# Kernel optimization log

Measured on AMD Instinct MI355X. Metric: run time of the kernel, lower is better.

The kernel has to match this reference:

```python
import jax, jax.numpy as jnp
import numpy as np

B, T, DM, H = 4, 2048, 1024, 16
D = DM // H  # head_dim = 64


def setup_inputs() -> dict:
    key = jax.random.key(0)
    ks = jax.random.split(key, 10)
    s = 0.02
    return {
        "query": jax.random.normal(ks[0], (B, T, DM), jnp.float32),
        "key": jax.random.normal(ks[1], (B, T, DM), jnp.float32),
        "value": jax.random.normal(ks[2], (B, T, DM), jnp.float32),
        "Wq": jax.random.normal(ks[3], (DM, DM), jnp.float32) * s,
        "bq": jnp.zeros((DM,), jnp.float32),
        "Wk": jax.random.normal(ks[4], (DM, DM), jnp.float32) * s,
        "bk": jnp.zeros((DM,), jnp.float32),
        "Wv": jax.random.normal(ks[5], (DM, DM), jnp.float32) * s,
        "bv": jnp.zeros((DM,), jnp.float32),
        "Wo": jax.random.normal(ks[6], (DM, DM), jnp.float32) * s,
        "bo": jnp.zeros((DM,), jnp.float32),
        "gate_w": jax.random.normal(ks[7], (H, D, D), jnp.float32) * s,
        "gate_b": jax.random.normal(ks[8], (H, D), jnp.float32),
    }


def _split_heads(x):
    # (B, T, DM) -> (B, H, T, D)
    b, t, _ = x.shape
    return x.reshape(b, t, H, D).transpose(0, 2, 1, 3)


def reference(query, key, value, Wq, bq, Wk, bk, Wv, bv, Wo, bo, gate_w, gate_b):
    q = _split_heads(query @ Wq + bq)   # (B,H,T,D)
    k = _split_heads(key @ Wk + bk)
    v = _split_heads(value @ Wv + bv)
    scale = 1.0 / jnp.sqrt(jnp.asarray(D, q.dtype))
    scores = jnp.einsum("bhqd,bhkd->bhqk", q, k) * scale  # (B,H,Tq,Tk)
    attn = jax.nn.softmax(scores, axis=-1)
    y = jnp.einsum("bhqk,bhkd->bhqd", attn, v)            # (B,H,T,D)
    # per-head elementwise gating: sigmoid(W_h y + b_h)
    gate = jax.nn.sigmoid(jnp.einsum("bhtd,hde->bhte", y, gate_w) + gate_b[None, :, None, :])
    y = y * gate
    y = y.transpose(0, 2, 1, 3).reshape(y.shape[0], y.shape[2], H * D)  # merge heads
    return y @ Wo + bo
```

## Files before the change

### kernel.cpp

```cpp
#include <hip/hip_runtime.h>
#include <stdint.h>

typedef unsigned short u16;
typedef uint32_t u32;
typedef __attribute__((ext_vector_type(8))) short bf16x8;
typedef __attribute__((ext_vector_type(4))) float f32x4;
typedef __attribute__((ext_vector_type(4))) u32 u32x4;

__device__ __forceinline__ u16 f2b(float x) {
  union { float f; uint32_t u; } v; v.f = x;
  uint32_t u = v.u;
  return (u16)((u + 0x7fffu + ((u >> 16) & 1u)) >> 16);
}

__device__ __forceinline__ float fexp2(float x) {
  float r;
  asm("v_exp_f32 %0, %1" : "=v"(r) : "v"(x));
  return r;
}

__device__ __forceinline__ u32 cvtpk(float lo, float hi) {
  u32 r;
  asm("v_cvt_pk_bf16_f32 %0, %1, %2" : "=v"(r) : "v"(lo), "v"(hi));
  return r;
}

__device__ __forceinline__ void gload_lds16(const void* g, void* l) {
  __builtin_amdgcn_global_load_lds(
      (const __attribute__((address_space(1))) void*)g,
      (__attribute__((address_space(3))) void*)l, 16, 0, 0);
}

__global__ __launch_bounds__(256) void cvt3_f32_bf16(const float* __restrict__ q,
                                                     const float* __restrict__ k,
                                                     const float* __restrict__ v,
                                                     u16* __restrict__ xq,
                                                     u16* __restrict__ xk,
                                                     u16* __restrict__ xv, int n4) {
  int idx = blockIdx.x * 256 + threadIdx.x;
  if (idx >= n4) return;
  const int z = blockIdx.y;
  const float* in = z == 0 ? q : z == 1 ? k : v;
  u16* out = z == 0 ? xq : z == 1 ? xk : xv;
  float4 vv = ((const float4*)in)[idx];
  ushort4 o;
  o.x = f2b(vv.x); o.y = f2b(vv.y); o.z = f2b(vv.z); o.w = f2b(vv.w);
  ((ushort4*)out)[idx] = o;
}

__global__ __launch_bounds__(256) void transpose_cvt4(const float* __restrict__ w0,
                                                      const float* __restrict__ w1,
                                                      const float* __restrict__ w2,
                                                      const float* __restrict__ w3,
                                                      u16* __restrict__ o0,
                                                      u16* __restrict__ o1,
                                                      u16* __restrict__ o2,
                                                      u16* __restrict__ o3) {
  __shared__ float t[64][65];
  const int z = blockIdx.z;
  const float* inp = z == 0 ? w0 : z == 1 ? w1 : z == 2 ? w2 : w3;
  u16* outp = z == 0 ? o0 : z == 1 ? o1 : z == 2 ? o2 : o3;
  int r0 = blockIdx.x * 64, c0 = blockIdx.y * 64;
  for (int i = 0; i < 16; ++i) {
    int idx = i * 256 + threadIdx.x;
    int r = idx >> 6, c = idx & 63;
    t[r][c] = inp[(size_t)(r0 + r) * 1024 + (c0 + c)];
  }
  __syncthreads();
  for (int i = 0; i < 16; ++i) {
    int idx = i * 256 + threadIdx.x;
    int c = idx >> 6, r = idx & 63;
    outp[(size_t)(c0 + c) * 1024 + (r0 + r)] = f2b(t[r][c]);
  }
}

__global__ __launch_bounds__(256) void transpose_gate(const float* __restrict__ in,
                                                      u16* __restrict__ out) {
  __shared__ float t[64][65];
  const float* inp = in + (size_t)blockIdx.z * 4096;
  u16* outp = out + (size_t)blockIdx.z * 4096;
  for (int i = 0; i < 16; ++i) {
    int idx = i * 256 + threadIdx.x;
    int r = idx >> 6, c = idx & 63;
    t[r][c] = inp[(size_t)r * 64 + c];
  }
  __syncthreads();
  for (int i = 0; i < 16; ++i) {
    int idx = i * 256 + threadIdx.x;
    int c = idx >> 6, r = idx & 63;
    outp[(size_t)c * 64 + r] = f2b(t[r][c]);
  }
}

template <int MODE>
__device__ __forceinline__ void gemm_body(const u16* __restrict__ A,
                                          const u16* __restrict__ Bt,
                                          const float* __restrict__ bias,
                                          void* __restrict__ Cout,
                                          int M, int N, int K, float scale,
                                          u16* lA, u16* lB) {
  const int tid = threadIdx.x;
  const int wave = tid >> 6, lane = tid & 63;
  const int l15 = lane & 15, l4 = lane >> 4;
  const int wr = (wave >> 1) * 64, wc = (wave & 1) * 64;
  const int bm = blockIdx.x, bn = blockIdx.y;
  f32x4 acc[4][4];
  for (int a = 0; a < 4; ++a)
    for (int b = 0; b < 4; ++b)
      for (int j = 0; j < 4; ++j) acc[a][b][j] = 0.f;
  const u16* Ab = A + (size_t)bm * 128 * K;
  const u16* Bb = Bt + (size_t)bn * 128 * K;
  for (int kt = 0; kt < K; kt += 64) {
    __syncthreads();
#pragma unroll
    for (int i = 0; i < 4; ++i) {
      int p = i * 256 + tid;
      int r = p >> 3, kc = p & 7, skc = kc ^ (r & 7);
      gload_lds16(Ab + (size_t)r * K + kt + skc * 8, &lA[p * 8]);
    }
#pragma unroll
    for (int i = 0; i < 4; ++i) {
      int p = i * 256 + tid;
      int r = p >> 3, kc = p & 7, skc = kc ^ (r & 7);
      gload_lds16(Bb + (size_t)r * K + kt + skc * 8, &lB[p * 8]);
    }
    __syncthreads();
#pragma unroll
    for (int kk = 0; kk < 2; ++kk) {
      const int kch = kk * 4 + l4;
      bf16x8 af[4], bfr[4];
#pragma unroll
      for (int mt = 0; mt < 4; ++mt) {
        int r = wr + mt * 16 + l15;
        af[mt] = *(const bf16x8*)&lA[r * 64 + ((kch ^ (r & 7)) << 3)];
      }
#pragma unroll
      for (int nt = 0; nt < 4; ++nt) {
        int r = wc + nt * 16 + l15;
        bfr[nt] = *(const bf16x8*)&lB[r * 64 + ((kch ^ (r & 7)) << 3)];
      }
      __builtin_amdgcn_s_setprio(1);
#pragma unroll
      for (int mt = 0; mt < 4; ++mt)
#pragma unroll
        for (int nt = 0; nt < 4; ++nt)
          acc[mt][nt] = __builtin_amdgcn_mfma_f32_16x16x32_bf16(af[mt], bfr[nt],
                                                                acc[mt][nt], 0, 0, 0);
      __builtin_amdgcn_s_setprio(0);
    }
  }
  float bval[4];
#pragma unroll
  for (int nt = 0; nt < 4; ++nt) bval[nt] = bias[bn * 128 + wc + nt * 16 + l15];
#pragma unroll
  for (int mt = 0; mt < 4; ++mt) {
#pragma unroll
    for (int nt = 0; nt < 4; ++nt) {
      int n = bn * 128 + wc + nt * 16 + l15;
#pragma unroll
      for (int i = 0; i < 4; ++i) {
        int m = bm * 128 + wr + mt * 16 + l4 * 4 + i;
        float v = acc[mt][nt][i] + bval[nt];
        if constexpr (MODE == 0) {
          ((float*)Cout)[(size_t)m * N + n] = v;
        } else {
          int bb = m >> 11, t = m & 2047, hh = n >> 6, d = n & 63;
          ((u16*)Cout)[(((size_t)bb * 16 + hh) * 2048 + t) * 64 + d] = f2b(v * scale);
        }
      }
    }
  }
}

__global__ __launch_bounds__(256) void gemm_qkv(const u16* __restrict__ Xq,
                                                const u16* __restrict__ Xk,
                                                const u16* __restrict__ Xv,
                                                const u16* __restrict__ WqT,
                                                const u16* __restrict__ WkT,
                                                const u16* __restrict__ WvT,
                                                const float* __restrict__ bq,
                                                const float* __restrict__ bk,
                                                const float* __restrict__ bv,
                                                u16* __restrict__ Qb,
                                                u16* __restrict__ Kb,
                                                u16* __restrict__ Vtm, float qscale) {
  __shared__ __align__(16) u16 lA[128 * 64];
  __shared__ __align__(16) u16 lB[128 * 64];
  const int z = blockIdx.z;
  const u16* A = z == 0 ? Xq : z == 1 ? Xk : Xv;
  const u16* Bt = z == 0 ? WqT : z == 1 ? WkT : WvT;
  const float* bias = z == 0 ? bq : z == 1 ? bk : bv;
  u16* C = z == 0 ? Qb : z == 1 ? Kb : Vtm;
  float scale = z == 0 ? qscale : 1.0f;
  gemm_body<1>(A, Bt, bias, C, 8192, 1024, 1024, scale, lA, lB);
}

__global__ __launch_bounds__(256) void gemm_out(const u16* __restrict__ A,
                                                const u16* __restrict__ Bt,
                                                const float* __restrict__ bias,
                                                float* __restrict__ C) {
  __shared__ __align__(16) u16 lA[128 * 64];
  __shared__ __align__(16) u16 lB[128 * 64];
  gemm_body<0>(A, Bt, bias, C, 8192, 1024, 1024, 1.0f, lA, lB);
}

__global__ __launch_bounds__(256) void transpose_v_bf16(const u16* __restrict__ in,
                                                        u16* __restrict__ out) {
  __shared__ u16 t[64][72];
  int t0 = blockIdx.x * 64;
  const u16* inp = in + (size_t)blockIdx.y * 2048 * 64;
  u16* outp = out + (size_t)blockIdx.y * 64 * 2048;
  for (int i = 0; i < 16; ++i) {
    int idx = i * 256 + threadIdx.x;
    int r = idx >> 6, c = idx & 63;
    t[r][c] = inp[(size_t)(t0 + r) * 64 + c];
  }
  __syncthreads();
  for (int i = 0; i < 16; ++i) {
    int idx = i * 256 + threadIdx.x;
    int d = idx >> 6, tt = idx & 63;
    outp[(size_t)d * 2048 + (t0 + tt)] = t[tt][d];
  }
}

__global__ __launch_bounds__(256) void attn_fused(const u16* __restrict__ Qb,
                                                  const u16* __restrict__ Kb,
                                                  const u16* __restrict__ Vt,
                                                  const u16* __restrict__ GwT,
                                                  const float* __restrict__ gate_b,
                                                  u16* __restrict__ Yg) {
  __shared__ __align__(16) u16 lK[2][64 * 64];
  __shared__ __align__(16) u16 lV[2][64 * 64];
  const int tid = threadIdx.x;
  const int w = tid >> 6, lane = tid & 63;
  const int l15 = lane & 15, l4 = lane >> 4;
  const int qt = blockIdx.x, bh = blockIdx.y;
  const int b = bh >> 4, h = bh & 15;

  const u16* Qg = Qb + ((size_t)bh * 2048 + qt * 64 + w * 16 + l15) * 64;
  bf16x8 qf[2];
  qf[0] = *(const bf16x8*)(Qg + l4 * 8);
  qf[1] = *(const bf16x8*)(Qg + 32 + l4 * 8);

  const bf16x8 ones = {0x3F80, 0x3F80, 0x3F80, 0x3F80, 0x3F80, 0x3F80, 0x3F80, 0x3F80};

  f32x4 acc[4];
  f32x4 lsum;
#pragma unroll
  for (int nt = 0; nt < 4; ++nt)
#pragma unroll
    for (int j = 0; j < 4; ++j) acc[nt][j] = 0.f;
#pragma unroll
  for (int j = 0; j < 4; ++j) lsum[j] = 0.f;

  const u16* Kg = Kb + (size_t)bh * 2048 * 64;
  const u16* Vg = Vt + (size_t)bh * 64 * 2048;

  auto STAGE = [&](int buf, int tile) {
#pragma unroll
    for (int i = 0; i < 2; ++i) {
      int p = i * 256 + tid;
      int r = p >> 3, kc = p & 7, skc = kc ^ (r & 7);
      int sr = ((r << 1) & 0x38) | ((r >> 3) & 4) | (r & 3);
      gload_lds16(Kg + (size_t)(tile * 64 + sr) * 64 + skc * 8, &lK[buf][p * 8]);
      gload_lds16(Vg + (size_t)r * 2048 + tile * 64 + skc * 8, &lV[buf][p * 8]);
    }
  };

  STAGE(0, 0);
  __syncthreads();

  for (int kv = 0; kv < 32; ++kv) {
    const int cur = kv & 1;
    if (kv + 1 < 32) STAGE(cur ^ 1, kv + 1);

    f32x4 s[4];
#pragma unroll
    for (int nt = 0; nt < 4; ++nt)
#pragma unroll
      for (int j = 0; j < 4; ++j) s[nt][j] = 0.f;
    __builtin_amdgcn_s_setprio(1);
#pragma unroll
    for (int kk = 0; kk < 2; ++kk) {
      const int kch = kk * 4 + l4;
#pragma unroll
      for (int nt = 0; nt < 4; ++nt) {
        int r = nt * 16 + l15;
        bf16x8 kf = *(const bf16x8*)&lK[cur][r * 64 + ((kch ^ (r & 7)) << 3)];
        s[nt] = __builtin_amdgcn_mfma_f32_16x16x32_bf16(kf, qf[kk], s[nt], 0, 0, 0);
      }
    }
    __builtin_amdgcn_s_setprio(0);

    u32 pk[4][2];
#pragma unroll
    for (int nt = 0; nt < 4; ++nt) {
      float p0 = fexp2(s[nt][0]), p1 = fexp2(s[nt][1]);
      float p2 = fexp2(s[nt][2]), p3 = fexp2(s[nt][3]);
      pk[nt][0] = cvtpk(p0, p1);
      pk[nt][1] = cvtpk(p2, p3);
    }
    bf16x8 pf[2];
    {
      union { u32x4 u; bf16x8 bv; } c0, c1;
      c0.u = (u32x4){pk[0][0], pk[0][1], pk[2][0], pk[2][1]};
      c1.u = (u32x4){pk[1][0], pk[1][1], pk[3][0], pk[3][1]};
      pf[0] = c0.bv;
      pf[1] = c1.bv;
    }

    __builtin_amdgcn_s_setprio(1);
    lsum = __builtin_amdgcn_mfma_f32_16x16x32_bf16(ones, pf[0], lsum, 0, 0, 0);
    lsum = __builtin_amdgcn_mfma_f32_16x16x32_bf16(ones, pf[1], lsum, 0, 0, 0);
#pragma unroll
    for (int kk = 0; kk < 2; ++kk) {
      const int kch = kk * 4 + l4;
#pragma unroll
      for (int nt = 0; nt < 4; ++nt) {
        int r = nt * 16 + l15;
        bf16x8 vf = *(const bf16x8*)&lV[cur][r * 64 + ((kch ^ (r & 7)) << 3)];
        acc[nt] = __builtin_amdgcn_mfma_f32_16x16x32_bf16(vf, pf[kk], acc[nt], 0, 0, 0);
      }
    }
    __builtin_amdgcn_s_setprio(0);
    __syncthreads();
  }

  float inv = 1.f / lsum[0];
  float y[4][4];
#pragma unroll
  for (int nt = 0; nt < 4; ++nt)
#pragma unroll
    for (int i = 0; i < 4; ++i) y[nt][i] = acc[nt][i] * inv;

  bf16x8 gwf[2][4];
  {
    const u16* g = GwT + (size_t)h * 4096;
#pragma unroll
    for (int kk = 0; kk < 2; ++kk)
#pragma unroll
      for (int et = 0; et < 4; ++et)
        gwf[kk][et] = *(const bf16x8*)(g + (et * 16 + l15) * 64 + (kk * 4 + l4) * 8);
  }

  u32* ws32 = (u32*)&lK[0][0] + w * 1024;
  const int rsw = (l15 & 7) << 2;
#pragma unroll
  for (int nt = 0; nt < 4; ++nt) {
    u32 y0 = cvtpk(y[nt][0], y[nt][1]);
    u32 y1 = cvtpk(y[nt][2], y[nt][3]);
    int col = (nt * 8 + l4 * 2) ^ rsw;
    *(uint64_t*)(ws32 + l15 * 64 + col) = ((uint64_t)y1 << 32) | y0;
  }
  asm volatile("s_waitcnt lgkmcnt(0)" ::: "memory");
  bf16x8 yf[2];
  yf[0] = *(const bf16x8*)(ws32 + l15 * 64 + ((l4 * 4) ^ rsw));
  yf[1] = *(const bf16x8*)(ws32 + l15 * 64 + ((16 + l4 * 4) ^ rsw));

  f32x4 g4[4];
#pragma unroll
  for (int et = 0; et < 4; ++et)
#pragma unroll
    for (int j = 0; j < 4; ++j) g4[et][j] = 0.f;
#pragma unroll
  for (int kk = 0; kk < 2; ++kk)
#pragma unroll
    for (int et = 0; et < 4; ++et)
      g4[et] = __builtin_amdgcn_mfma_f32_16x16x32_bf16(gwf[kk][et], yf[kk], g4[et], 0, 0, 0);

  const float* gb = gate_b + h * 64;
  u32 ok[4][2];
#pragma unroll
  for (int et = 0; et < 4; ++et) {
    float o[4];
#pragma unroll
    for (int i = 0; i < 4; ++i) {
      float gv = g4[et][i] + gb[et * 16 + l4 * 4 + i];
      float sg = 1.f / (1.f + __expf(-gv));
      o[i] = y[et][i] * sg;
    }
    ok[et][0] = cvtpk(o[0], o[1]);
    ok[et][1] = cvtpk(o[2], o[3]);
  }
  asm volatile("s_waitcnt lgkmcnt(0)" ::: "memory");
#pragma unroll
  for (int et = 0; et < 4; ++et) {
    int col = (et * 8 + l4 * 2) ^ rsw;
    *(uint64_t*)(ws32 + l15 * 64 + col) = ((uint64_t)ok[et][1] << 32) | ok[et][0];
  }
  asm volatile("s_waitcnt lgkmcnt(0)" ::: "memory");
  {
    int rr = lane >> 2, c = lane & 3;
    int rs2 = (rr & 7) << 2;
    u32x4 d0 = *(const u32x4*)(ws32 + rr * 64 + ((c * 4) ^ rs2));
    u32x4 d1 = *(const u32x4*)(ws32 + rr * 64 + (((c + 4) * 4) ^ rs2));
    size_t row = (size_t)b * 2048 + qt * 64 + w * 16 + rr;
    u32* og = (u32*)(Yg + row * 1024 + h * 64);
    *(u32x4*)(og + c * 4) = d0;
    *(u32x4*)(og + (c + 4) * 4) = d1;
  }
}

extern "C" void kernel_launch(void* const* d_in, const int* in_sizes, int n_in,
                              void* d_out, int out_size, void* d_ws, size_t ws_size,
                              hipStream_t stream) {
  (void)in_sizes; (void)n_in; (void)out_size; (void)ws_size;
  const float* query  = (const float*)d_in[0];
  const float* key    = (const float*)d_in[1];
  const float* value  = (const float*)d_in[2];
  const float* Wq     = (const float*)d_in[3];
  const float* bq     = (const float*)d_in[4];
  const float* Wk     = (const float*)d_in[5];
  const float* bk     = (const float*)d_in[6];
  const float* Wv     = (const float*)d_in[7];
  const float* bv     = (const float*)d_in[8];
  const float* Wo     = (const float*)d_in[9];
  const float* bo     = (const float*)d_in[10];
  const float* gate_w = (const float*)d_in[11];
  const float* gate_b = (const float*)d_in[12];

  const size_t XN = (size_t)8192 * 1024;
  const size_t WN = (size_t)1024 * 1024;
  char* ws = (char*)d_ws;
  size_t off = 0;
  auto nxt = [&](size_t bytes) {
    char* p = ws + off;
    off += (bytes + 255) & ~(size_t)255;
    return p;
  };
  u16* Xq  = (u16*)nxt(XN * 2);
  u16* Xk  = (u16*)nxt(XN * 2);
  u16* Xv  = (u16*)nxt(XN * 2);
  u16* WqT = (u16*)nxt(WN * 2);
  u16* WkT = (u16*)nxt(WN * 2);
  u16* WvT = (u16*)nxt(WN * 2);
  u16* WoT = (u16*)nxt(WN * 2);
  u16* GwT = (u16*)nxt((size_t)16 * 64 * 64 * 2);
  u16* Qb  = (u16*)nxt(XN * 2);
  u16* Kb  = (u16*)nxt(XN * 2);
  u16* Vtm = (u16*)nxt(XN * 2);
  u16* Vtr = (u16*)nxt(XN * 2);
  u16* Yg  = (u16*)nxt(XN * 2);

  int n4 = (int)(XN / 4);
  cvt3_f32_bf16<<<dim3(n4 / 256, 3), 256, 0, stream>>>(query, key, value, Xq, Xk, Xv, n4);
  transpose_cvt4<<<dim3(16, 16, 4), 256, 0, stream>>>(Wq, Wk, Wv, Wo, WqT, WkT, WvT, WoT);
  transpose_gate<<<dim3(1, 1, 16), 256, 0, stream>>>(gate_w, GwT);

  gemm_qkv<<<dim3(64, 8, 3), 256, 0, stream>>>(Xq, Xk, Xv, WqT, WkT, WvT, bq, bk, bv,
                                               Qb, Kb, Vtm, 0.125f * 1.44269504f);
  transpose_v_bf16<<<dim3(32, 64), 256, 0, stream>>>(Vtm, Vtr);
  attn_fused<<<dim3(32, 64), 256, 0, stream>>>(Qb, Kb, Vtr, GwT, gate_b, Yg);
  gemm_out<<<dim3(64, 8), 256, 0, stream>>>(Yg, WoT, bo, (float*)d_out);
}
```

Measured before the change: 232.9 us.

## Compute V transposed directly in QKV GEMM and restructure attention K/V staging

The V projection is now computed as WvT·Xv^T (swapped operands, new MODE 2 epilogue with per-row bias) so it is written directly in the transposed head-major layout. This removes the separate transpose_v_bf16 kernel and its intermediate buffer. The attention loop is also rewritten with macros, a single LDS array, precomputed fragment pointers and pointer-increment staging, and it is unrolled by two over the double buffer to cut address arithmetic. The transposed epilogue writes strided 2-byte stores along t, which may be poorly coalesced.

```diff
diff --git a/kernel.cpp b/kernel.cpp
--- a/kernel.cpp
+++ b/kernel.cpp
@@ -98,12 +98,11 @@
                                           const float* __restrict__ bias,
                                           void* __restrict__ Cout,
                                           int M, int N, int K, float scale,
-                                          u16* lA, u16* lB) {
+                                          u16* lA, u16* lB, int bm, int bn) {
   const int tid = threadIdx.x;
   const int wave = tid >> 6, lane = tid & 63;
   const int l15 = lane & 15, l4 = lane >> 4;
   const int wr = (wave >> 1) * 64, wc = (wave & 1) * 64;
-  const int bm = blockIdx.x, bn = blockIdx.y;
   f32x4 acc[4][4];
   for (int a = 0; a < 4; ++a)
     for (int b = 0; b < 4; ++b)
@@ -150,8 +149,17 @@
     }
   }
   float bval[4];
-#pragma unroll
-  for (int nt = 0; nt < 4; ++nt) bval[nt] = bias[bn * 128 + wc + nt * 16 + l15];
+  float bvalm[4][4];
+  if constexpr (MODE == 2) {
+#pragma unroll
+    for (int mt = 0; mt < 4; ++mt)
+#pragma unroll
+      for (int i = 0; i < 4; ++i)
+        bvalm[mt][i] = bias[bm * 128 + wr + mt * 16 + l4 * 4 + i];
+  } else {
+#pragma unroll
+    for (int nt = 0; nt < 4; ++nt) bval[nt] = bias[bn * 128 + wc + nt * 16 + l15];
+  }
 #pragma unroll
   for (int mt = 0; mt < 4; ++mt) {
 #pragma unroll
@@ -160,12 +168,16 @@
 #pragma unroll
       for (int i = 0; i < 4; ++i) {
         int m = bm * 128 + wr + mt * 16 + l4 * 4 + i;
-        float v = acc[mt][nt][i] + bval[nt];
         if constexpr (MODE == 0) {
-          ((float*)Cout)[(size_t)m * N + n] = v;
-        } else {
+          ((float*)Cout)[(size_t)m * N + n] = acc[mt][nt][i] + bval[nt];
+        } else if constexpr (MODE == 1) {
+          float v = acc[mt][nt][i] + bval[nt];
           int bb = m >> 11, t = m & 2047, hh = n >> 6, d = n & 63;
           ((u16*)Cout)[(((size_t)bb * 16 + hh) * 2048 + t) * 64 + d] = f2b(v * scale);
+        } else {
+          float v = acc[mt][nt][i] + bvalm[mt][i];
+          int bb = n >> 11, t = n & 2047, hh = m >> 6, d = m & 63;
+          ((u16*)Cout)[(((size_t)bb * 16 + hh) * 64 + d) * 2048 + t] = f2b(v);
         }
       }
     }
@@ -183,16 +195,22 @@
                                                 const float* __restrict__ bv,
                                                 u16* __restrict__ Qb,
                                                 u16* __restrict__ Kb,
-                                                u16* __restrict__ Vtm, float qscale) {
+                                                u16* __restrict__ Vtr, float qscale) {
   __shared__ __align__(16) u16 lA[128 * 64];
   __shared__ __align__(16) u16 lB[128 * 64];
   const int z = blockIdx.z;
-  const u16* A = z == 0 ? Xq : z == 1 ? Xk : Xv;
-  const u16* Bt = z == 0 ? WqT : z == 1 ? WkT : WvT;
-  const float* bias = z == 0 ? bq : z == 1 ? bk : bv;
-  u16* C = z == 0 ? Qb : z == 1 ? Kb : Vtm;
-  float scale = z == 0 ? qscale : 1.0f;
-  gemm_body<1>(A, Bt, bias, C, 8192, 1024, 1024, scale, lA, lB);
+  if (z == 2) {
+    gemm_body<2>(WvT, Xv, bv, Vtr, 1024, 8192, 1024, 1.0f, lA, lB,
+                 blockIdx.y, blockIdx.x);
+  } else {
+    const u16* A = z == 0 ? Xq : Xk;
+    const u16* Bt = z == 0 ? WqT : WkT;
+    const float* bias = z == 0 ? bq : bk;
+    u16* C = z == 0 ? Qb : Kb;
+    float scale = z == 0 ? qscale : 1.0f;
+    gemm_body<1>(A, Bt, bias, C, 8192, 1024, 1024, scale, lA, lB,
+                 blockIdx.x, blockIdx.y);
+  }
 }
 
 __global__ __launch_bounds__(256) void gemm_out(const u16* __restrict__ A,
@@ -201,26 +219,8 @@
                                                 float* __restrict__ C) {
   __shared__ __align__(16) u16 lA[128 * 64];
   __shared__ __align__(16) u16 lB[128 * 64];
-  gemm_body<0>(A, Bt, bias, C, 8192, 1024, 1024, 1.0f, lA, lB);
-}
-
-__global__ __launch_bounds__(256) void transpose_v_bf16(const u16* __restrict__ in,
-                                                        u16* __restrict__ out) {
-  __shared__ u16 t[64][72];
-  int t0 = blockIdx.x * 64;
-  const u16* inp = in + (size_t)blockIdx.y * 2048 * 64;
-  u16* outp = out + (size_t)blockIdx.y * 64 * 2048;
-  for (int i = 0; i < 16; ++i) {
-    int idx = i * 256 + threadIdx.x;
-    int r = idx >> 6, c = idx & 63;
-    t[r][c] = inp[(size_t)(t0 + r) * 64 + c];
-  }
-  __syncthreads();
-  for (int i = 0; i < 16; ++i) {
-    int idx = i * 256 + threadIdx.x;
-    int d = idx >> 6, tt = idx & 63;
-    outp[(size_t)d * 2048 + (t0 + tt)] = t[tt][d];
-  }
+  gemm_body<0>(A, Bt, bias, C, 8192, 1024, 1024, 1.0f, lA, lB,
+               blockIdx.x, blockIdx.y);
 }
 
 __global__ __launch_bounds__(256) void attn_fused(const u16* __restrict__ Qb,
@@ -229,8 +229,7 @@
                                                   const u16* __restrict__ GwT,
                                                   const float* __restrict__ gate_b,
                                                   u16* __restrict__ Yg) {
-  __shared__ __align__(16) u16 lK[2][64 * 64];
-  __shared__ __align__(16) u16 lV[2][64 * 64];
+  __shared__ __align__(16) u16 lds[16384];
   const int tid = threadIdx.x;
   const int w = tid >> 6, lane = tid & 63;
   const int l15 = lane & 15, l4 = lane >> 4;
@@ -238,11 +237,11 @@
   const int b = bh >> 4, h = bh & 15;
 
   const u16* Qg = Qb + ((size_t)bh * 2048 + qt * 64 + w * 16 + l15) * 64;
-  bf16x8 qf[2];
-  qf[0] = *(const bf16x8*)(Qg + l4 * 8);
-  qf[1] = *(const bf16x8*)(Qg + 32 + l4 * 8);
+  bf16x8 qf0 = *(const bf16x8*)(Qg + l4 * 8);
+  bf16x8 qf1 = *(const bf16x8*)(Qg + 32 + l4 * 8);
 
   const bf16x8 ones = {0x3F80, 0x3F80, 0x3F80, 0x3F80, 0x3F80, 0x3F80, 0x3F80, 0x3F80};
+  const f32x4 fz = {0.f, 0.f, 0.f, 0.f};
 
   f32x4 acc[4];
   f32x4 lsum;
@@ -253,78 +252,75 @@
 #pragma unroll
   for (int j = 0; j < 4; ++j) lsum[j] = 0.f;
 
-  const u16* Kg = Kb + (size_t)bh * 2048 * 64;
-  const u16* Vg = Vt + (size_t)bh * 64 * 2048;
-
-  auto STAGE = [&](int buf, int tile) {
-#pragma unroll
-    for (int i = 0; i < 2; ++i) {
-      int p = i * 256 + tid;
-      int r = p >> 3, kc = p & 7, skc = kc ^ (r & 7);
-      int sr = ((r << 1) & 0x38) | ((r >> 3) & 4) | (r & 3);
-      gload_lds16(Kg + (size_t)(tile * 64 + sr) * 64 + skc * 8, &lK[buf][p * 8]);
-      gload_lds16(Vg + (size_t)r * 2048 + tile * 64 + skc * 8, &lV[buf][p * 8]);
-    }
-  };
-
-  STAGE(0, 0);
+  const u16* f0 = lds + l15 * 64 + ((l4 ^ (l15 & 7)) << 3);
+  const u16* f1 = lds + l15 * 64 + (((4 + l4) ^ (l15 & 7)) << 3);
+
+  const int r0 = tid >> 3, kc0 = tid & 7, skc = kc0 ^ (r0 & 7);
+  const int sr = ((r0 << 1) & 0x38) | ((r0 >> 3) & 4) | (r0 & 3);
+  const u16* kp  = Kb + (size_t)bh * 131072 + (size_t)sr * 64 + skc * 8;
+  const u16* kp2 = kp + 256;
+  const u16* vp  = Vt + (size_t)bh * 131072 + (size_t)r0 * 2048 + skc * 8;
+  const u16* vp2 = vp + (size_t)32 * 2048;
+  u16* dK = lds + tid * 8;
+  u16* dV = lds + 8192 + tid * 8;
+
+#define STAGE(c)                                                     \
+  do {                                                               \
+    gload_lds16(kp, dK + (c)*4096);                                  \
+    gload_lds16(kp2, dK + (c)*4096 + 2048);                          \
+    gload_lds16(vp, dV + (c)*4096);                                  \
+    gload_lds16(vp2, dV + (c)*4096 + 2048);                          \
+    kp += 4096; kp2 += 4096; vp += 64; vp2 += 64;                    \
+  } while (0)
+
+#define COMPUTE(c)                                                            \
+  do {                                                                        \
+    f32x4 s[4];                                                               \
+    __builtin_amdgcn_s_setprio(1);                                            \
+    _Pragma("unroll") for (int nt = 0; nt < 4; ++nt) {                        \
+      bf16x8 kf = *(const bf16x8*)(f0 + (c)*4096 + nt * 1024);                \
+      s[nt] = __builtin_amdgcn_mfma_f32_16x16x32_bf16(kf, qf0, fz, 0, 0, 0);  \
+    }                                                                         \
+    _Pragma("unroll") for (int nt = 0; nt < 4; ++nt) {                        \
+      bf16x8 kf = *(const bf16x8*)(f1 + (c)*4096 + nt * 1024);                \
+      s[nt] = __builtin_amdgcn_mfma_f32_16x16x32_bf16(kf, qf1, s[nt], 0, 0, 0);\
+    }                                                                         \
+    __builtin_amdgcn_s_setprio(0);                                           \
+    union { u32x4 u; bf16x8 bv; } c0, c1;                                     \
+    c0.u[0] = cvtpk(fexp2(s[0][0]), fexp2(s[0][1]));                          \
+    c0.u[1] = cvtpk(fexp2(s[0][2]), fexp2(s[0][3]));                          \
+    c0.u[2] = cvtpk(fexp2(s[2][0]), fexp2(s[2][1]));                          \
+    c0.u[3] = cvtpk(fexp2(s[2][2]), fexp2(s[2][3]));                          \
+    c1.u[0] = cvtpk(fexp2(s[1][0]), fexp2(s[1][1]));                          \
+    c1.u[1] = cvtpk(fexp2(s[1][2]), fexp2(s[1][3]));                          \
+    c1.u[2] = cvtpk(fexp2(s[3][0]), fexp2(s[3][1]));                          \
+    c1.u[3] = cvtpk(fexp2(s[3][2]), fexp2(s[3][3]));                          \
+    __builtin_amdgcn_s_setprio(1);                                           \
+    lsum = __builtin_amdgcn_mfma_f32_16x16x32_bf16(ones, c0.bv, lsum, 0, 0, 0);\
+    lsum = __builtin_amdgcn_mfma_f32_16x16x32_bf16(ones, c1.bv, lsum, 0, 0, 0);\
+    _Pragma("unroll") for (int nt = 0; nt < 4; ++nt) {                        \
+      bf16x8 vf = *(const bf16x8*)(f0 + 8192 + (c)*4096 + nt * 1024);         \
+      acc[nt] = __builtin_amdgcn_mfma_f32_16x16x32_bf16(vf, c0.bv, acc[nt], 0, 0, 0);\
+    }                                                                         \
+    _Pragma("unroll") for (int nt = 0; nt < 4; ++nt) {                        \
+      bf16x8 vf = *(const bf16x8*)(f1 + 8192 + (c)*4096 + nt * 1024);         \
+      acc[nt] = __builtin_amdgcn_mfma_f32_16x16x32_bf16(vf, c1.bv, acc[nt], 0, 0, 0);\
+    }                                                                         \
+    __builtin_amdgcn_s_setprio(0);                                           \
+  } while (0)
+
+  STAGE(0);
   __syncthreads();
-
-  for (int kv = 0; kv < 32; ++kv) {
-    const int cur = kv & 1;
-    if (kv + 1 < 32) STAGE(cur ^ 1, kv + 1);
-
-    f32x4 s[4];
-#pragma unroll
-    for (int nt = 0; nt < 4; ++nt)
-#pragma unroll
-      for (int j = 0; j < 4; ++j) s[nt][j] = 0.f;
-    __builtin_amdgcn_s_setprio(1);
-#pragma unroll
-    for (int kk = 0; kk < 2; ++kk) {
-      const int kch = kk * 4 + l4;
-#pragma unroll
-      for (int nt = 0; nt < 4; ++nt) {
-        int r = nt * 16 + l15;
-        bf16x8 kf = *(const bf16x8*)&lK[cur][r * 64 + ((kch ^ (r & 7)) << 3)];
-        s[nt] = __builtin_amdgcn_mfma_f32_16x16x32_bf16(kf, qf[kk], s[nt], 0, 0, 0);
-      }
-    }
-    __builtin_amdgcn_s_setprio(0);
-
-    u32 pk[4][2];
-#pragma unroll
-    for (int nt = 0; nt < 4; ++nt) {
-      float p0 = fexp2(s[nt][0]), p1 = fexp2(s[nt][1]);
-      float p2 = fexp2(s[nt][2]), p3 = fexp2(s[nt][3]);
-      pk[nt][0] = cvtpk(p0, p1);
-      pk[nt][1] = cvtpk(p2, p3);
-    }
-    bf16x8 pf[2];
-    {
-      union { u32x4 u; bf16x8 bv; } c0, c1;
-      c0.u = (u32x4){pk[0][0], pk[0][1], pk[2][0], pk[2][1]};
-      c1.u = (u32x4){pk[1][0], pk[1][1], pk[3][0], pk[3][1]};
-      pf[0] = c0.bv;
-      pf[1] = c1.bv;
-    }
-
-    __builtin_amdgcn_s_setprio(1);
-    lsum = __builtin_amdgcn_mfma_f32_16x16x32_bf16(ones, pf[0], lsum, 0, 0, 0);
-    lsum = __builtin_amdgcn_mfma_f32_16x16x32_bf16(ones, pf[1], lsum, 0, 0, 0);
-#pragma unroll
-    for (int kk = 0; kk < 2; ++kk) {
-      const int kch = kk * 4 + l4;
-#pragma unroll
-      for (int nt = 0; nt < 4; ++nt) {
-        int r = nt * 16 + l15;
-        bf16x8 vf = *(const bf16x8*)&lV[cur][r * 64 + ((kch ^ (r & 7)) << 3)];
-        acc[nt] = __builtin_amdgcn_mfma_f32_16x16x32_bf16(vf, pf[kk], acc[nt], 0, 0, 0);
-      }
-    }
-    __builtin_amdgcn_s_setprio(0);
+  for (int it = 0; it < 16; ++it) {
+    STAGE(1);
+    COMPUTE(0);
     __syncthreads();
-  }
+    if (it < 15) STAGE(0);
+    COMPUTE(1);
+    __syncthreads();
+  }
+#undef STAGE
+#undef COMPUTE
 
   float inv = 1.f / lsum[0];
   float y[4][4];
@@ -343,7 +339,7 @@
         gwf[kk][et] = *(const bf16x8*)(g + (et * 16 + l15) * 64 + (kk * 4 + l4) * 8);
   }
 
-  u32* ws32 = (u32*)&lK[0][0] + w * 1024;
+  u32* ws32 = (u32*)lds + w * 1024;
   const int rsw = (l15 & 7) << 2;
 #pragma unroll
   for (int nt = 0; nt < 4; ++nt) {
@@ -438,7 +434,6 @@
   u16* GwT = (u16*)nxt((size_t)16 * 64 * 64 * 2);
   u16* Qb  = (u16*)nxt(XN * 2);
   u16* Kb  = (u16*)nxt(XN * 2);
-  u16* Vtm = (u16*)nxt(XN * 2);
   u16* Vtr = (u16*)nxt(XN * 2);
   u16* Yg  = (u16*)nxt(XN * 2);
 
@@ -448,8 +443,7 @@
   transpose_gate<<<dim3(1, 1, 16), 256, 0, stream>>>(gate_w, GwT);
 
   gemm_qkv<<<dim3(64, 8, 3), 256, 0, stream>>>(Xq, Xk, Xv, WqT, WkT, WvT, bq, bk, bv,
-                                               Qb, Kb, Vtm, 0.125f * 1.44269504f);
-  transpose_v_bf16<<<dim3(32, 64), 256, 0, stream>>>(Vtm, Vtr);
+                                               Qb, Kb, Vtr, 0.125f * 1.44269504f);
   attn_fused<<<dim3(32, 64), 256, 0, stream>>>(Qb, Kb, Vtr, GwT, gate_b, Yg);
   gemm_out<<<dim3(64, 8), 256, 0, stream>>>(Yg, WoT, bo, (float*)d_out);
 }
```

Result: faster. 222.3 us (-4.6%).
